# Optimization experiments

Measured on AMD Instinct MI355X. Metric: run time of the kernel, lower is better.

## Reference

```python
import jax, jax.numpy as jnp
import numpy as np

BATCH = 256
VOCAB = 128000


def setup_inputs() -> dict:
    key = jax.random.key(0)
    k1, k2, k3 = jax.random.split(key, 3)
    logits = jax.random.normal(k1, (BATCH, VOCAB), dtype=jnp.float32)
    # temperatures in (0.1, 1.0); a fraction set to 0 to exercise the greedy path
    temps = jax.random.uniform(k2, (BATCH,), dtype=jnp.float32, minval=0.1, maxval=1.0)
    greedy_sel = jax.random.uniform(jax.random.fold_in(k2, 1), (BATCH,)) < 0.25
    temperatures = jnp.where(greedy_sel, 0.0, temps)
    # exponential(1) noise, matching torch.empty_like(probs).exponential_(1)
    noise = jax.random.exponential(k3, (BATCH, VOCAB), dtype=jnp.float32)
    return {"logits": logits, "temperatures": temperatures, "noise": noise}


def reference(logits, temperatures, noise):
    # faithful to Sampler.forward_opt / forward_original (Gumbel-max via exp noise)
    logits = logits.astype(jnp.float32)
    greedy_tokens = jnp.argmax(logits, axis=-1)
    # guard temp==0 to avoid nan in the (discarded) sampled branch
    safe_t = jnp.where(temperatures == 0, 1.0, temperatures)
    scaled = logits / safe_t[:, None]
    probs = jax.nn.softmax(scaled, axis=-1)
    sample_tokens = jnp.argmax(probs / noise, axis=-1)
    return jnp.where(temperatures == 0, greedy_tokens, sample_tokens)
```

## Files before the change

### kernel.cpp

```cpp
#include <hip/hip_runtime.h>
#include <hip/hip_bf16.h>

#define VOCAB 128000
#define BATCH 256
#define NTHREADS 1024

__global__ __launch_bounds__(NTHREADS) void sampler_kernel(
    const float* __restrict__ logits,
    const float* __restrict__ temps,
    const float* __restrict__ noise,
    int* __restrict__ out)
{
    const int row  = blockIdx.x;
    const int tid  = threadIdx.x;
    const float t  = temps[row];
    const bool greedy = (t == 0.0f);
    const float invT  = greedy ? 1.0f : (1.0f / t);

    const float4* __restrict__ lg4 = (const float4*)(logits + (size_t)row * VOCAB);
    const float4* __restrict__ nz4 = (const float4*)(noise  + (size_t)row * VOCAB);
    const int nvec = VOCAB / 4;

    float best = -INFINITY;
    int   bidx = 0x7fffffff;

    if (greedy) {
        for (int v = tid; v < nvec; v += NTHREADS) {
            float4 l = lg4[v];
            int base = v * 4;
            if (l.x > best) { best = l.x; bidx = base;     }
            if (l.y > best) { best = l.y; bidx = base + 1; }
            if (l.z > best) { best = l.z; bidx = base + 2; }
            if (l.w > best) { best = l.w; bidx = base + 3; }
        }
    } else {
        for (int v = tid; v < nvec; v += NTHREADS) {
            float4 l = lg4[v];
            float4 n = nz4[v];
            int base = v * 4;
            float vx = l.x * invT - __logf(n.x);
            float vy = l.y * invT - __logf(n.y);
            float vz = l.z * invT - __logf(n.z);
            float vw = l.w * invT - __logf(n.w);
            if (vx > best) { best = vx; bidx = base;     }
            if (vy > best) { best = vy; bidx = base + 1; }
            if (vz > best) { best = vz; bidx = base + 2; }
            if (vw > best) { best = vw; bidx = base + 3; }
        }
    }

    #pragma unroll
    for (int off = 32; off > 0; off >>= 1) {
        float ov = __shfl_xor(best, off, 64);
        int   oi = __shfl_xor(bidx, off, 64);
        if (ov > best || (ov == best && oi < bidx)) { best = ov; bidx = oi; }
    }

    __shared__ float sv[NTHREADS / 64];
    __shared__ int   si[NTHREADS / 64];
    const int wave = tid >> 6;
    const int lane = tid & 63;
    if (lane == 0) { sv[wave] = best; si[wave] = bidx; }
    __syncthreads();

    if (tid == 0) {
        float b  = sv[0];
        int   bi = si[0];
        #pragma unroll
        for (int w = 1; w < NTHREADS / 64; ++w) {
            float ov = sv[w]; int oi = si[w];
            if (ov > b || (ov == b && oi < bi)) { b = ov; bi = oi; }
        }
        out[row] = bi;
    }
}

extern "C" void kernel_launch(void* const* d_in, const int* in_sizes, int n_in,
                              void* d_out, int out_size, void* d_ws, size_t ws_size,
                              hipStream_t stream) {
    const float* logits = (const float*)d_in[0];
    const float* temps  = (const float*)d_in[1];
    const float* noise  = (const float*)d_in[2];
    int* out = (int*)d_out;

    sampler_kernel<<<BATCH, NTHREADS, 0, stream>>>(logits, temps, noise, out);
}
```

Baseline: 268.6 us.

## Split each row's argmax across vocab segments with a second-pass reduction

Each row is now split into 8 vocab segments, each handled by a 256-thread block, so the grid grows from 256 blocks to 2048. Each block writes its best value and index, packed into a sortable 64-bit key, to workspace, and a small second kernel reduces the 8 partials per row. The goal is better load balance and occupancy across the GPU's compute units, since greedy rows read half the data and the old one-block-per-row grid left some units idle. The cost is an extra kernel launch and a small workspace round-trip.

```diff
diff --git a/kernel.cpp b/kernel.cpp
--- a/kernel.cpp
+++ b/kernel.cpp
@@ -1,43 +1,54 @@
 #include <hip/hip_runtime.h>
 #include <hip/hip_bf16.h>
 
-#define VOCAB 128000
-#define BATCH 256
-#define NTHREADS 1024
+#define VOCAB   128000
+#define BATCH   256
+#define SEGS    8
+#define SEGLEN  (VOCAB / SEGS)
+#define TPB     256
 
-__global__ __launch_bounds__(NTHREADS) void sampler_kernel(
+__device__ inline unsigned long long packvi(float v, int idx) {
+    unsigned u = __float_as_uint(v);
+    u = (u & 0x80000000u) ? ~u : (u | 0x80000000u);
+    return ((unsigned long long)u << 32) | (unsigned)(~idx);
+}
+
+__global__ __launch_bounds__(TPB) void seg_kernel(
     const float* __restrict__ logits,
     const float* __restrict__ temps,
     const float* __restrict__ noise,
-    int* __restrict__ out)
+    unsigned long long* __restrict__ ws)
 {
-    const int row  = blockIdx.x;
-    const int tid  = threadIdx.x;
-    const float t  = temps[row];
+    const int seg = blockIdx.x;
+    const int row = blockIdx.y;
+    const int tid = threadIdx.x;
+
+    const float t = temps[row];
     const bool greedy = (t == 0.0f);
     const float invT  = greedy ? 1.0f : (1.0f / t);
 
-    const float4* __restrict__ lg4 = (const float4*)(logits + (size_t)row * VOCAB);
-    const float4* __restrict__ nz4 = (const float4*)(noise  + (size_t)row * VOCAB);
-    const int nvec = VOCAB / 4;
+    const int base0 = seg * SEGLEN;
+    const float4* __restrict__ lg4 = (const float4*)(logits + (size_t)row * VOCAB + base0);
+    const float4* __restrict__ nz4 = (const float4*)(noise  + (size_t)row * VOCAB + base0);
+    const int nvec = SEGLEN / 4;
 
     float best = -INFINITY;
     int   bidx = 0x7fffffff;
 
     if (greedy) {
-        for (int v = tid; v < nvec; v += NTHREADS) {
+        for (int v = tid; v < nvec; v += TPB) {
             float4 l = lg4[v];
-            int base = v * 4;
+            int base = base0 + v * 4;
             if (l.x > best) { best = l.x; bidx = base;     }
             if (l.y > best) { best = l.y; bidx = base + 1; }
             if (l.z > best) { best = l.z; bidx = base + 2; }
             if (l.w > best) { best = l.w; bidx = base + 3; }
         }
     } else {
-        for (int v = tid; v < nvec; v += NTHREADS) {
+        for (int v = tid; v < nvec; v += TPB) {
             float4 l = lg4[v];
             float4 n = nz4[v];
-            int base = v * 4;
+            int base = base0 + v * 4;
             float vx = l.x * invT - __logf(n.x);
             float vy = l.y * invT - __logf(n.y);
             float vz = l.z * invT - __logf(n.z);
@@ -56,8 +67,8 @@
         if (ov > best || (ov == best && oi < bidx)) { best = ov; bidx = oi; }
     }
 
-    __shared__ float sv[NTHREADS / 64];
-    __shared__ int   si[NTHREADS / 64];
+    __shared__ float sv[TPB / 64];
+    __shared__ int   si[TPB / 64];
     const int wave = tid >> 6;
     const int lane = tid & 63;
     if (lane == 0) { sv[wave] = best; si[wave] = bidx; }
@@ -67,12 +78,26 @@
         float b  = sv[0];
         int   bi = si[0];
         #pragma unroll
-        for (int w = 1; w < NTHREADS / 64; ++w) {
+        for (int w = 1; w < TPB / 64; ++w) {
             float ov = sv[w]; int oi = si[w];
             if (ov > b || (ov == b && oi < bi)) { b = ov; bi = oi; }
         }
-        out[row] = bi;
+        ws[(size_t)row * SEGS + seg] = packvi(b, bi);
     }
+}
+
+__global__ __launch_bounds__(BATCH) void fin_kernel(
+    const unsigned long long* __restrict__ ws,
+    int* __restrict__ out)
+{
+    const int r = threadIdx.x;
+    unsigned long long m = ws[(size_t)r * SEGS];
+    #pragma unroll
+    for (int s = 1; s < SEGS; ++s) {
+        unsigned long long v = ws[(size_t)r * SEGS + s];
+        if (v > m) m = v;
+    }
+    out[r] = (int)(~(unsigned)(m & 0xffffffffull));
 }
 
 extern "C" void kernel_launch(void* const* d_in, const int* in_sizes, int n_in,
@@ -82,6 +107,9 @@
     const float* temps  = (const float*)d_in[1];
     const float* noise  = (const float*)d_in[2];
     int* out = (int*)d_out;
+    unsigned long long* ws = (unsigned long long*)d_ws;
 
-    sampler_kernel<<<BATCH, NTHREADS, 0, stream>>>(logits, temps, noise, out);
+    dim3 grid(SEGS, BATCH);
+    seg_kernel<<<grid, TPB, 0, stream>>>(logits, temps, noise, ws);
+    fin_kernel<<<1, BATCH, 0, stream>>>(ws, out);
 }
```

New measurement: 274.2 us. +2.1%, slower.
